# Optimization experiments

Hardware: AMD Instinct MI355X
Metric: run time of the kernel (lower is better)

The kernel has to match this reference:

```python
import jax, jax.numpy as jnp
import numpy as np

THRESHOLD_FRAC = 0.1  # default `threshold` kwarg in RingLoss.forward


def _l2_normalize(x):
    # matches torch.nn.functional.normalize(x, p=2, dim=1, eps=1e-12)
    n = jnp.linalg.norm(x, axis=1, keepdims=True)
    return x / jnp.maximum(n, 1e-12)


def setup_inputs() -> dict:
    key = jax.random.key(0)
    k1, k2, k3 = jax.random.split(key, 3)
    N, D = 4096, 512
    h1 = jax.random.normal(k1, (N, D), dtype=jnp.float32)
    h2 = jax.random.normal(k2, (N, D), dtype=jnp.float32)
    y = jax.random.randint(k3, (N,), 0, 100)  # class labels
    tau = jnp.asarray(0.5, dtype=jnp.float32)  # contrastive temperature
    return {"h1": h1, "h2": h2, "y": y, "tau": tau}


def reference(h1, h2, y, tau):
    # NOTE: in the original module, `y` is only used to build false_neg_mask /
    # false_neg_cnt, which are dead values (never used in the returned loss).
    # The loss itself depends only on h1, h2, tau, threshold.
    N = h1.shape[0]
    t = int(N * THRESHOLD_FRAC)  # static ring cutoff

    h1n = _l2_normalize(h1)
    h2n = _l2_normalize(h2)

    s12 = h1n @ h2n.T  # [N, N] cross-view similarity
    s11 = h1n @ h1n.T  # [N, N]
    s22 = h2n @ h2n.T  # [N, N]

    neg1 = jnp.concatenate([s11, s12], axis=1)    # [N, 2N]
    neg2 = jnp.concatenate([s12.T, s22], axis=1)  # [N, 2N]

    # sort descending per row, keep the middle "ring" [t : 2N - t]
    neg1 = jnp.sort(neg1, axis=1)[:, ::-1][:, t:2 * N - t]
    neg2 = jnp.sort(neg2, axis=1)[:, ::-1][:, t:2 * N - t]

    f = lambda x: jnp.exp(x / tau)
    pos = f(jnp.diagonal(s12))      # [N]
    n1 = f(neg1).sum(axis=1)        # [N]
    n2 = f(neg2).sum(axis=1)        # [N]

    loss = 0.5 * (-jnp.log(pos / n1) - jnp.log(pos / n2))
    return loss.mean()
```

## Files before the change

### kernel.cpp

```cpp
#include <hip/hip_runtime.h>


typedef unsigned short u16;
typedef __bf16 bf16x8 __attribute__((ext_vector_type(8)));
typedef float f32x4 __attribute__((ext_vector_type(4)));
typedef u16 u16x8 __attribute__((ext_vector_type(8)));

#define NROW 8192
#define NHALF 4096
#define DIM 512
#define RING_T 409
#define TH_HI 0.05f
#define TH_LO -0.05f
#define CAP 3072

__device__ inline u16 f2bf(float f) {
  unsigned u = __builtin_bit_cast(unsigned, f);
  unsigned r = (u + 0x7fffu + ((u >> 16) & 1u)) >> 16;
  return (u16)r;
}
__device__ inline float bf2f(u16 h) {
  unsigned u = ((unsigned)h) << 16;
  return __builtin_bit_cast(float, u);
}
__device__ inline unsigned sortkey(unsigned b) {
  return (b & 0x8000u) ? (~b & 0xFFFFu) : (b | 0x8000u);
}
__device__ inline float key2val(unsigned k) {
  unsigned b = (k & 0x8000u) ? (k ^ 0x8000u) : (~k & 0xFFFFu);
  return bf2f((u16)b);
}

__device__ inline float block_sum(float x, volatile float* s4, int t) {
  #pragma unroll
  for (int off = 32; off > 0; off >>= 1) x += __shfl_down(x, off);
  __syncthreads();
  if ((t & 63) == 0) s4[t >> 6] = x;
  __syncthreads();
  return s4[0] + s4[1] + s4[2] + s4[3];
}

__global__ __launch_bounds__(256) void normalize_k(const float* __restrict__ h1,
                                                   const float* __restrict__ h2,
                                                   u16* __restrict__ G) {
  const int r = blockIdx.x;
  const int t = threadIdx.x;
  const float* src = (r < NHALF) ? (h1 + (size_t)r * DIM) : (h2 + (size_t)(r - NHALF) * DIM);
  float2 x = *(const float2*)(src + (t << 1));
  __shared__ float s4[4];
  float tot = block_sum(x.x * x.x + x.y * x.y, s4, t);
  float scale = 1.0f / fmaxf(sqrtf(tot), 1e-12f);
  unsigned pk = (unsigned)f2bf(x.x * scale) | ((unsigned)f2bf(x.y * scale) << 16);
  *(unsigned*)(G + (size_t)r * DIM + (t << 1)) = pk;
}

__global__ __launch_bounds__(256) void diag_k(const float* __restrict__ h1,
                                              const float* __restrict__ h2,
                                              float* __restrict__ accums) {
  const int i = blockIdx.x, t = threadIdx.x;
  float2 a = *(const float2*)(h1 + (size_t)i * DIM + (t << 1));
  float2 b = *(const float2*)(h2 + (size_t)i * DIM + (t << 1));
  __shared__ float s4[4];
  float S11 = block_sum(a.x * a.x + a.y * a.y, s4, t);
  float S22 = block_sum(b.x * b.x + b.y * b.y, s4, t);
  float S12 = block_sum(a.x * b.x + a.y * b.y, s4, t);
  if (t == 0) {
    float d = S12 / (fmaxf(sqrtf(S11), 1e-12f) * fmaxf(sqrtf(S22), 1e-12f));
    atomicAdd(&accums[1], d);
  }
}

#define BK 32

__device__ inline void gload_lds16(const u16* g, u16* lds_base) {
  __builtin_amdgcn_global_load_lds(
      (const __attribute__((address_space(1))) void*)g,
      (__attribute__((address_space(3))) void*)lds_base, 16, 0, 0);
}

__global__ __launch_bounds__(256) void gram_gemm(const u16* __restrict__ G,
                                                 u16* __restrict__ S,
                                                 int row0) {
  __shared__ u16 As[128 * BK];
  __shared__ u16 Bs[128 * BK];
  const int t = threadIdx.x;
  const int lane = t & 63;
  const int wave = t >> 6;
  const int wm = wave >> 1, wn = wave & 1;
  const int brow = row0 + (blockIdx.y << 7), bcol = blockIdx.x << 7;
  const int fr = lane & 15, fg = lane >> 4;

  const int srow = lane >> 2;
  const int scol = (lane & 3) << 3;
  const int chA0 = wave, chA1 = wave + 4;

  f32x4 acc[4][4] = {};

  for (int ks = 0; ks < DIM; ks += BK) {
    __syncthreads();
    gload_lds16(G + (size_t)(brow + (chA0 << 4) + srow) * DIM + ks + scol, As + (chA0 << 9));
    gload_lds16(G + (size_t)(brow + (chA1 << 4) + srow) * DIM + ks + scol, As + (chA1 << 9));
    gload_lds16(G + (size_t)(bcol + (chA0 << 4) + srow) * DIM + ks + scol, Bs + (chA0 << 9));
    gload_lds16(G + (size_t)(bcol + (chA1 << 4) + srow) * DIM + ks + scol, Bs + (chA1 << 9));
    __syncthreads();

    bf16x8 af[4], bfr[4];
    #pragma unroll
    for (int m = 0; m < 4; ++m)
      af[m] = __builtin_bit_cast(bf16x8,
          *(const u16x8*)(&As[(((wm << 6) + (m << 4) + fr) << 5) + (fg << 3)]));
    #pragma unroll
    for (int n = 0; n < 4; ++n)
      bfr[n] = __builtin_bit_cast(bf16x8,
          *(const u16x8*)(&Bs[(((wn << 6) + (n << 4) + fr) << 5) + (fg << 3)]));
    #pragma unroll
    for (int m = 0; m < 4; ++m)
      #pragma unroll
      for (int n = 0; n < 4; ++n)
        acc[m][n] = __builtin_amdgcn_mfma_f32_16x16x32_bf16(af[m], bfr[n], acc[m][n], 0, 0, 0);
  }

  #pragma unroll
  for (int m = 0; m < 4; ++m)
    #pragma unroll
    for (int n = 0; n < 4; ++n) {
      int lrow = (blockIdx.y << 7) + (wm << 6) + (m << 4) + (fg << 2);
      int col = bcol + (wn << 6) + (n << 4) + fr;
      #pragma unroll
      for (int j = 0; j < 4; ++j)
        S[(size_t)(lrow + j) * NROW + col] = f2bf(acc[m][n][j]);
    }
}

__global__ __launch_bounds__(256) void ring_k(const u16* __restrict__ S,
                                              const float* __restrict__ taup,
                                              float* __restrict__ accums) {
  __shared__ u16 listH[CAP];
  __shared__ u16 listL[CAP];
  __shared__ unsigned lens[2];
  __shared__ unsigned ured[2][4];
  __shared__ float fred[4][4];
  const int t = threadIdx.x;
  const int w = t >> 6, lane = t & 63;
  const int r = blockIdx.x;
  const float se = (1.0f / taup[0]) * 1.44269504f;

  if (t < 2) lens[t] = 0;
  __syncthreads();

  const u16* row = S + (size_t)r * NROW;
  u16x8 u[4];
  #pragma unroll
  for (int q = 0; q < 4; ++q)
    u[q] = *(const u16x8*)(row + (((q << 8) + t) << 3));

  float eTot = 0.0f;
  #pragma unroll
  for (int q = 0; q < 4; ++q)
    #pragma unroll
    for (int j = 0; j < 8; ++j) {
      unsigned b = u[q][j];
      float v = bf2f((u16)b);
      eTot += __builtin_amdgcn_exp2f(v * se);
      bool ph = v > TH_HI;
      bool pl = v < TH_LO;
      unsigned long long mh = __ballot(ph);
      unsigned long long ml = __ballot(pl);
      if (mh) {
        int leader = __ffsll((long long)mh) - 1;
        unsigned base = 0;
        if (lane == leader) base = atomicAdd(&lens[0], (unsigned)__popcll(mh));
        base = __shfl(base, leader);
        if (ph) {
          unsigned idx = base + (unsigned)__popcll(mh & ((1ull << lane) - 1ull));
          if (idx < CAP) listH[idx] = (u16)sortkey(b);
        }
      }
      if (ml) {
        int leader = __ffsll((long long)ml) - 1;
        unsigned base = 0;
        if (lane == leader) base = atomicAdd(&lens[1], (unsigned)__popcll(ml));
        base = __shfl(base, leader);
        if (pl) {
          unsigned idx = base + (unsigned)__popcll(ml & ((1ull << lane) - 1ull));
          if (idx < CAP) listL[idx] = (u16)sortkey(b);
        }
      }
    }
  __syncthreads();
  const int lenH = (int)min(lens[0], (unsigned)CAP);
  const int lenL = (int)min(lens[1], (unsigned)CAP);

  unsigned loH = 0, hiH = 0xFFFFu;
  unsigned loL = 0, hiL = 0xFFFFu;
  #pragma unroll 1
  for (int it = 0; it < 16; ++it) {
    unsigned midH = (loH + hiH) >> 1;
    unsigned midL = (loL + hiL + 1) >> 1;
    unsigned cpk = 0;
    for (int i = t; i < lenH; i += 256) cpk += (listH[i] > midH) ? 0x10000u : 0u;
    for (int i = t; i < lenL; i += 256) cpk += (listL[i] < midL) ? 1u : 0u;
    #pragma unroll
    for (int off = 32; off > 0; off >>= 1) cpk += __shfl_down(cpk, off);
    if (lane == 0) ured[it & 1][w] = cpk;
    __syncthreads();
    unsigned tot = ured[it & 1][0] + ured[it & 1][1] + ured[it & 1][2] + ured[it & 1][3];
    if ((tot >> 16) >= RING_T) loH = midH + 1; else hiH = midH;
    if ((tot & 0xFFFFu) >= RING_T) hiL = midL - 1; else loL = midL;
  }
  const unsigned kH = hiH, kL = loL;

  float tsum = 0.0f, bsum = 0.0f;
  unsigned cpk = 0;
  for (int i = t; i < lenH; i += 256) {
    unsigned k = listH[i];
    if (k > kH) { tsum += __builtin_amdgcn_exp2f(key2val(k) * se); cpk += 0x10000u; }
  }
  for (int i = t; i < lenL; i += 256) {
    unsigned k = listL[i];
    if (k < kL) { bsum += __builtin_amdgcn_exp2f(key2val(k) * se); cpk += 1u; }
  }
  float fpk = __builtin_bit_cast(float, cpk);
  #pragma unroll
  for (int off = 32; off > 0; off >>= 1) {
    eTot += __shfl_down(eTot, off);
    tsum += __shfl_down(tsum, off);
    bsum += __shfl_down(bsum, off);
    cpk += __builtin_bit_cast(unsigned, __shfl_down(__builtin_bit_cast(float, cpk), off));
  }
  (void)fpk;
  if (lane == 0) {
    fred[w][0] = eTot; fred[w][1] = tsum; fred[w][2] = bsum;
    fred[w][3] = __builtin_bit_cast(float, cpk);
  }
  __syncthreads();

  if (t == 0) {
    float E = 0, T = 0, B = 0; unsigned C = 0;
    #pragma unroll
    for (int k = 0; k < 4; ++k) {
      E += fred[k][0]; T += fred[k][1]; B += fred[k][2];
      C += __builtin_bit_cast(unsigned, fred[k][3]);
    }
    unsigned cgt = C >> 16, clt = C & 0xFFFFu;
    float top = T + (float)(RING_T - (int)cgt) * __builtin_amdgcn_exp2f(key2val(kH) * se);
    float bot = B + (float)(RING_T - (int)clt) * __builtin_amdgcn_exp2f(key2val(kL) * se);
    float ringv = E - top - bot;
    atomicAdd(&accums[0], 0.5f * __logf(ringv));
  }
}

__global__ void init_k(float* accums) {
  if (threadIdx.x < 2) accums[threadIdx.x] = 0.0f;
}

__global__ void final_k(const float* __restrict__ accums,
                        const float* __restrict__ taup,
                        float* __restrict__ out) {
  out[0] = (accums[0] - accums[1] / taup[0]) * (1.0f / (float)NHALF);
}

extern "C" void kernel_launch(void* const* d_in, const int* in_sizes, int n_in,
                              void* d_out, int out_size, void* d_ws, size_t ws_size,
                              hipStream_t stream) {
  const float* h1 = (const float*)d_in[0];
  const float* h2 = (const float*)d_in[1];
  const float* taup = (const float*)d_in[3];
  float* out = (float*)d_out;

  char* ws = (char*)d_ws;
  u16* G = (u16*)ws;
  float* accums = (float*)(ws + (size_t)8 * 1024 * 1024);
  u16* Schunk = (u16*)(ws + (size_t)8 * 1024 * 1024 + 256);

  size_t avail = (ws_size > (size_t)8 * 1024 * 1024 + 256)
                     ? ws_size - (size_t)8 * 1024 * 1024 - 256 : 0;
  long long rpc = (long long)(avail / ((size_t)NROW * 2));
  rpc = (rpc / 128) * 128;
  if (rpc < 128) rpc = 128;
  if (rpc > NROW) rpc = NROW;

  hipLaunchKernelGGL(init_k, dim3(1), dim3(64), 0, stream, accums);
  hipLaunchKernelGGL(normalize_k, dim3(NROW), dim3(256), 0, stream, h1, h2, G);
  hipLaunchKernelGGL(diag_k, dim3(NHALF), dim3(256), 0, stream, h1, h2, accums);

  for (int r0 = 0; r0 < NROW; r0 += (int)rpc) {
    int rows = (int)((r0 + rpc <= NROW) ? rpc : (NROW - r0));
    hipLaunchKernelGGL(gram_gemm, dim3(64, rows >> 7), dim3(256), 0, stream,
                       G, Schunk, r0);
    hipLaunchKernelGGL(ring_k, dim3(rows), dim3(256), 0, stream,
                       Schunk, taup, accums);
  }

  hipLaunchKernelGGL(final_k, dim3(1), dim3(1), 0, stream, accums, taup, out);
}
```

Before: 382.8 us.

## Double-buffer Gram GEMM LDS loads and make ring selection register-resident

The Gram GEMM now double-buffers its LDS tiles, issuing the next K-slice's direct-to-LDS loads before computing on the current one, with explicit vmcnt waits and raw barriers. The ring kernel drops the thresholded LDS candidate lists and their atomics. It keeps all 32 values and exps per thread in registers and binary-searches the cutoff keys with ballot and popcount counts over the full row. This removes the compaction atomics and the CAP/threshold assumption, but adds per-iteration 32-element ballot loops and higher register pressure in the ring kernel.

```diff
diff --git a/kernel.cpp b/kernel.cpp
--- a/kernel.cpp
+++ b/kernel.cpp
@@ -10,9 +10,6 @@
 #define NHALF 4096
 #define DIM 512
 #define RING_T 409
-#define TH_HI 0.05f
-#define TH_LO -0.05f
-#define CAP 3072
 
 __device__ inline u16 f2bf(float f) {
   unsigned u = __builtin_bit_cast(unsigned, f);
@@ -22,9 +19,6 @@
 __device__ inline float bf2f(u16 h) {
   unsigned u = ((unsigned)h) << 16;
   return __builtin_bit_cast(float, u);
-}
-__device__ inline unsigned sortkey(unsigned b) {
-  return (b & 0x8000u) ? (~b & 0xFFFFu) : (b | 0x8000u);
 }
 __device__ inline float key2val(unsigned k) {
   unsigned b = (k & 0x8000u) ? (k ^ 0x8000u) : (~k & 0xFFFFu);
@@ -81,8 +75,8 @@
 __global__ __launch_bounds__(256) void gram_gemm(const u16* __restrict__ G,
                                                  u16* __restrict__ S,
                                                  int row0) {
-  __shared__ u16 As[128 * BK];
-  __shared__ u16 Bs[128 * BK];
+  __shared__ u16 As[2][128 * BK];
+  __shared__ u16 Bs[2][128 * BK];
   const int t = threadIdx.x;
   const int lane = t & 63;
   const int wave = t >> 6;
@@ -92,33 +86,53 @@
 
   const int srow = lane >> 2;
   const int scol = (lane & 3) << 3;
-  const int chA0 = wave, chA1 = wave + 4;
+  const int ch0 = wave, ch1 = wave + 4;
+
+  #define STAGE(p, ks)                                                                   \
+    do {                                                                                 \
+      gload_lds16(G + (size_t)(brow + (ch0 << 4) + srow) * DIM + (ks) + scol,            \
+                  &As[p][ch0 << 9]);                                                     \
+      gload_lds16(G + (size_t)(brow + (ch1 << 4) + srow) * DIM + (ks) + scol,            \
+                  &As[p][ch1 << 9]);                                                     \
+      gload_lds16(G + (size_t)(bcol + (ch0 << 4) + srow) * DIM + (ks) + scol,            \
+                  &Bs[p][ch0 << 9]);                                                     \
+      gload_lds16(G + (size_t)(bcol + (ch1 << 4) + srow) * DIM + (ks) + scol,            \
+                  &Bs[p][ch1 << 9]);                                                     \
+    } while (0)
 
   f32x4 acc[4][4] = {};
 
-  for (int ks = 0; ks < DIM; ks += BK) {
-    __syncthreads();
-    gload_lds16(G + (size_t)(brow + (chA0 << 4) + srow) * DIM + ks + scol, As + (chA0 << 9));
-    gload_lds16(G + (size_t)(brow + (chA1 << 4) + srow) * DIM + ks + scol, As + (chA1 << 9));
-    gload_lds16(G + (size_t)(bcol + (chA0 << 4) + srow) * DIM + ks + scol, Bs + (chA0 << 9));
-    gload_lds16(G + (size_t)(bcol + (chA1 << 4) + srow) * DIM + ks + scol, Bs + (chA1 << 9));
-    __syncthreads();
+  STAGE(0, 0);
+  #pragma unroll 2
+  for (int step = 0; step < 16; ++step) {
+    const int cur = step & 1;
+    if (step < 15) {
+      STAGE(cur ^ 1, (step + 1) << 5);
+      asm volatile("s_waitcnt vmcnt(4)" ::: "memory");
+    } else {
+      asm volatile("s_waitcnt vmcnt(0)" ::: "memory");
+    }
+    __builtin_amdgcn_s_barrier();
 
     bf16x8 af[4], bfr[4];
     #pragma unroll
     for (int m = 0; m < 4; ++m)
       af[m] = __builtin_bit_cast(bf16x8,
-          *(const u16x8*)(&As[(((wm << 6) + (m << 4) + fr) << 5) + (fg << 3)]));
+          *(const u16x8*)(&As[cur][(((wm << 6) + (m << 4) + fr) << 5) + (fg << 3)]));
     #pragma unroll
     for (int n = 0; n < 4; ++n)
       bfr[n] = __builtin_bit_cast(bf16x8,
-          *(const u16x8*)(&Bs[(((wn << 6) + (n << 4) + fr) << 5) + (fg << 3)]));
+          *(const u16x8*)(&Bs[cur][(((wn << 6) + (n << 4) + fr) << 5) + (fg << 3)]));
     #pragma unroll
     for (int m = 0; m < 4; ++m)
       #pragma unroll
       for (int n = 0; n < 4; ++n)
         acc[m][n] = __builtin_amdgcn_mfma_f32_16x16x32_bf16(af[m], bfr[n], acc[m][n], 0, 0, 0);
-  }
+
+    asm volatile("" ::: "memory");
+    __builtin_amdgcn_s_barrier();
+  }
+  #undef STAGE
 
   #pragma unroll
   for (int m = 0; m < 4; ++m)
@@ -135,103 +149,76 @@
 __global__ __launch_bounds__(256) void ring_k(const u16* __restrict__ S,
                                               const float* __restrict__ taup,
                                               float* __restrict__ accums) {
-  __shared__ u16 listH[CAP];
-  __shared__ u16 listL[CAP];
-  __shared__ unsigned lens[2];
-  __shared__ unsigned ured[2][4];
-  __shared__ float fred[4][4];
+  __shared__ unsigned redc[2][4];
+  __shared__ unsigned redc2[4];
+  __shared__ float redf[4][4];
   const int t = threadIdx.x;
   const int w = t >> 6, lane = t & 63;
   const int r = blockIdx.x;
   const float se = (1.0f / taup[0]) * 1.44269504f;
 
-  if (t < 2) lens[t] = 0;
-  __syncthreads();
-
   const u16* row = S + (size_t)r * NROW;
   u16x8 u[4];
   #pragma unroll
   for (int q = 0; q < 4; ++q)
     u[q] = *(const u16x8*)(row + (((q << 8) + t) << 3));
 
+  float v[32], e[32];
   float eTot = 0.0f;
   #pragma unroll
   for (int q = 0; q < 4; ++q)
     #pragma unroll
     for (int j = 0; j < 8; ++j) {
-      unsigned b = u[q][j];
-      float v = bf2f((u16)b);
-      eTot += __builtin_amdgcn_exp2f(v * se);
-      bool ph = v > TH_HI;
-      bool pl = v < TH_LO;
-      unsigned long long mh = __ballot(ph);
-      unsigned long long ml = __ballot(pl);
-      if (mh) {
-        int leader = __ffsll((long long)mh) - 1;
-        unsigned base = 0;
-        if (lane == leader) base = atomicAdd(&lens[0], (unsigned)__popcll(mh));
-        base = __shfl(base, leader);
-        if (ph) {
-          unsigned idx = base + (unsigned)__popcll(mh & ((1ull << lane) - 1ull));
-          if (idx < CAP) listH[idx] = (u16)sortkey(b);
-        }
-      }
-      if (ml) {
-        int leader = __ffsll((long long)ml) - 1;
-        unsigned base = 0;
-        if (lane == leader) base = atomicAdd(&lens[1], (unsigned)__popcll(ml));
-        base = __shfl(base, leader);
-        if (pl) {
-          unsigned idx = base + (unsigned)__popcll(ml & ((1ull << lane) - 1ull));
-          if (idx < CAP) listL[idx] = (u16)sortkey(b);
-        }
-      }
-    }
-  __syncthreads();
-  const int lenH = (int)min(lens[0], (unsigned)CAP);
-  const int lenL = (int)min(lens[1], (unsigned)CAP);
-
-  unsigned loH = 0, hiH = 0xFFFFu;
-  unsigned loL = 0, hiL = 0xFFFFu;
+      float x = bf2f((u16)u[q][j]);
+      float ex = __builtin_amdgcn_exp2f(x * se);
+      v[(q << 3) + j] = x;
+      e[(q << 3) + j] = ex;
+      eTot += ex;
+    }
+
+  unsigned loH = 0x3FFFu, hiH = 0xC000u;
+  unsigned loL = 0x3FFFu, hiL = 0xC000u;
   #pragma unroll 1
   for (int it = 0; it < 16; ++it) {
-    unsigned midH = (loH + hiH) >> 1;
-    unsigned midL = (loL + hiL + 1) >> 1;
-    unsigned cpk = 0;
-    for (int i = t; i < lenH; i += 256) cpk += (listH[i] > midH) ? 0x10000u : 0u;
-    for (int i = t; i < lenL; i += 256) cpk += (listL[i] < midL) ? 1u : 0u;
-    #pragma unroll
-    for (int off = 32; off > 0; off >>= 1) cpk += __shfl_down(cpk, off);
-    if (lane == 0) ured[it & 1][w] = cpk;
+    const unsigned midH = (loH + hiH) >> 1;
+    const unsigned midL = (loL + hiL) >> 1;
+    const float fH = key2val(midH), fL = key2val(midL);
+    unsigned cH = 0, cL = 0;
+    #pragma unroll
+    for (int i = 0; i < 32; ++i) {
+      cH += (unsigned)__popcll(__ballot(v[i] > fH));
+      cL += (unsigned)__popcll(__ballot(v[i] < fL));
+    }
+    if (lane == 0) redc[it & 1][w] = (cH << 16) | cL;
     __syncthreads();
-    unsigned tot = ured[it & 1][0] + ured[it & 1][1] + ured[it & 1][2] + ured[it & 1][3];
-    if ((tot >> 16) >= RING_T) loH = midH + 1; else hiH = midH;
-    if ((tot & 0xFFFFu) >= RING_T) hiL = midL - 1; else loL = midL;
-  }
-  const unsigned kH = hiH, kL = loL;
+    const unsigned tot = redc[it & 1][0] + redc[it & 1][1]
+                       + redc[it & 1][2] + redc[it & 1][3];
+    const unsigned CH = tot >> 16, CL = tot & 0xFFFFu;
+    if (hiH - loH > 1) { if (CH >= RING_T) loH = midH; else hiH = midH; }
+    if (hiL - loL > 1) { if (CL < RING_T) loL = midL; else hiL = midL; }
+  }
+  const float fH = key2val(hiH);
+  const float fL = key2val(loL);
 
   float tsum = 0.0f, bsum = 0.0f;
-  unsigned cpk = 0;
-  for (int i = t; i < lenH; i += 256) {
-    unsigned k = listH[i];
-    if (k > kH) { tsum += __builtin_amdgcn_exp2f(key2val(k) * se); cpk += 0x10000u; }
-  }
-  for (int i = t; i < lenL; i += 256) {
-    unsigned k = listL[i];
-    if (k < kL) { bsum += __builtin_amdgcn_exp2f(key2val(k) * se); cpk += 1u; }
-  }
-  float fpk = __builtin_bit_cast(float, cpk);
+  unsigned cgt = 0, clt = 0;
+  #pragma unroll
+  for (int i = 0; i < 32; ++i) {
+    const bool gh = v[i] > fH, lo = v[i] < fL;
+    cgt += (unsigned)__popcll(__ballot(gh));
+    clt += (unsigned)__popcll(__ballot(lo));
+    tsum += gh ? e[i] : 0.0f;
+    bsum += lo ? e[i] : 0.0f;
+  }
   #pragma unroll
   for (int off = 32; off > 0; off >>= 1) {
     eTot += __shfl_down(eTot, off);
     tsum += __shfl_down(tsum, off);
     bsum += __shfl_down(bsum, off);
-    cpk += __builtin_bit_cast(unsigned, __shfl_down(__builtin_bit_cast(float, cpk), off));
-  }
-  (void)fpk;
+  }
   if (lane == 0) {
-    fred[w][0] = eTot; fred[w][1] = tsum; fred[w][2] = bsum;
-    fred[w][3] = __builtin_bit_cast(float, cpk);
+    redf[w][0] = eTot; redf[w][1] = tsum; redf[w][2] = bsum;
+    redc2[w] = (cgt << 16) | clt;
   }
   __syncthreads();
 
@@ -239,14 +226,12 @@
     float E = 0, T = 0, B = 0; unsigned C = 0;
     #pragma unroll
     for (int k = 0; k < 4; ++k) {
-      E += fred[k][0]; T += fred[k][1]; B += fred[k][2];
-      C += __builtin_bit_cast(unsigned, fred[k][3]);
-    }
-    unsigned cgt = C >> 16, clt = C & 0xFFFFu;
-    float top = T + (float)(RING_T - (int)cgt) * __builtin_amdgcn_exp2f(key2val(kH) * se);
-    float bot = B + (float)(RING_T - (int)clt) * __builtin_amdgcn_exp2f(key2val(kL) * se);
-    float ringv = E - top - bot;
-    atomicAdd(&accums[0], 0.5f * __logf(ringv));
+      E += redf[k][0]; T += redf[k][1]; B += redf[k][2]; C += redc2[k];
+    }
+    const unsigned Cg = C >> 16, Cl = C & 0xFFFFu;
+    const float top = T + (float)(int)(RING_T - Cg) * __builtin_amdgcn_exp2f(fH * se);
+    const float bot = B + (float)(int)(RING_T - Cl) * __builtin_amdgcn_exp2f(fL * se);
+    atomicAdd(&accums[0], 0.5f * __logf(E - top - bot));
   }
 }
 
```

New measurement: 421.0 us. 10.0% more time.
